# Kernel optimization log

Measured on AMD Instinct MI355X. Metric: run time of the kernel, lower is better.

The kernel has to match this reference:

```python
import jax, jax.numpy as jnp
import numpy as np

B, C, H, W = 32, 512, 32, 32
HID, MEM = 256, 256


def setup_inputs() -> dict:
    key = jax.random.key(0)
    k1, k2, k3, k4, k5, k6 = jax.random.split(key, 6)
    x = jax.random.normal(k1, (B, C, H, W), dtype=jnp.float32)
    h = jax.random.normal(k2, (B, MEM), dtype=jnp.float32)
    # conv1: 1x1 conv, no bias -> weight [HID, C]
    W_conv1 = jax.random.normal(k3, (HID, C), dtype=jnp.float32) / np.sqrt(C)
    # linear1: memory_dim -> hidden_dim, with bias
    W_lin = jax.random.normal(k4, (HID, MEM), dtype=jnp.float32) / np.sqrt(MEM)
    b_lin = jax.random.normal(k5, (HID,), dtype=jnp.float32) * 0.01
    # attention_conv: 1x1 conv hidden->1, no bias -> weight [HID]
    W_attn = jax.random.normal(k6, (HID,), dtype=jnp.float32) / np.sqrt(HID)
    return {"x": x, "h": h, "W_conv1": W_conv1, "W_lin": W_lin,
            "b_lin": b_lin, "W_attn": W_attn}


def reference(x, h, W_conv1, W_lin, b_lin, W_attn):
    # x: [B,C,H,W], h: [B,MEM]
    x2 = x.reshape(x.shape[0], x.shape[1], -1)            # [B,C,HW]
    x3 = jnp.einsum('bchw,kc->bkhw', x, W_conv1)          # 1x1 conv -> [B,HID,H,W]
    h3 = (h @ W_lin.T + b_lin)[:, :, None, None]          # [B,HID,1,1] broadcast over H,W
    a1 = jnp.tanh(x3 + h3)                                # [B,HID,H,W]
    a2 = jnp.einsum('bkhw,k->bhw', a1, W_attn).reshape(x.shape[0], -1)  # [B,HW]
    a3 = jax.nn.softmax(a2, axis=1)                       # [B,HW]
    context = jnp.einsum('bcs,bs->bc', x2, a3)            # [B,C]
    return (a3, context)
```

## Files before the change

kernel.cpp:

```cpp
#include <hip/hip_runtime.h>
#include <hip/hip_bf16.h>
#include <cmath>


typedef __bf16 bf16;
typedef __attribute__((ext_vector_type(8))) __bf16 bf16x8;
typedef __attribute__((ext_vector_type(16))) float f32x16;

__global__ __launch_bounds__(256) void prep_kernel(const float* __restrict__ h,
                                                   const float* __restrict__ Wlin,
                                                   const float* __restrict__ blin,
                                                   const float* __restrict__ Wc,
                                                   float* __restrict__ h3,
                                                   bf16* __restrict__ Whi,
                                                   bf16* __restrict__ Wlo) {
    const int tid = threadIdx.x;
    if (blockIdx.x < 32) {
        const int b = blockIdx.x;
        __shared__ float hs[256];
        hs[tid] = h[b * 256 + tid];
        __syncthreads();
        const float4* wr = (const float4*)(Wlin + (size_t)tid * 256);
        float acc = blin[tid];
        #pragma unroll 8
        for (int q = 0; q < 64; ++q) {
            float4 w = wr[q];
            float4 hv = *(const float4*)&hs[q * 4];
            acc = fmaf(w.x, hv.x, fmaf(w.y, hv.y, fmaf(w.z, hv.z, fmaf(w.w, hv.w, acc))));
        }
        h3[b * 256 + tid] = acc;
    } else {
        const int e0 = (blockIdx.x - 32) * 2048 + tid * 8;
        float4 v0 = *(const float4*)(Wc + e0);
        float4 v1 = *(const float4*)(Wc + e0 + 4);
        float vs[8] = {v0.x, v0.y, v0.z, v0.w, v1.x, v1.y, v1.z, v1.w};
        bf16x8 vh, vl;
        #pragma unroll
        for (int j = 0; j < 8; ++j) {
            bf16 hi = (bf16)vs[j];
            float r = vs[j] - (float)hi;
            vh[j] = hi;
            vl[j] = (bf16)r;
        }
        *(bf16x8*)&Whi[e0] = vh;
        *(bf16x8*)&Wlo[e0] = vl;
    }
}

__global__ __launch_bounds__(256, 2) void fused_mfma(const float* __restrict__ x,
                                                     const bf16* __restrict__ Whi,
                                                     const bf16* __restrict__ Wlo,
                                                     const float* __restrict__ h3,
                                                     const float* __restrict__ Wattn,
                                                     float* __restrict__ a2) {
    __shared__ float xbuf[2][64 * 64];
    __shared__ bf16x8 fragB[16 * 64];
    __shared__ float red2[4 * 64];

    const int tid = threadIdx.x;
    const int bid = blockIdx.x;
    const int wk = (bid & 7) * 64 + (bid >> 3);
    const int b  = wk >> 4;
    const int s0 = (wk & 15) * 64;

    const int w  = tid >> 6;
    const int l  = tid & 63;
    const int h  = l >> 5;
    const int lr = l & 31;

    const float* xb = x + ((size_t)b << 19) + s0;

    const bf16* aphi[2];
    const bf16* aplo[2];
    #pragma unroll
    for (int mf = 0; mf < 2; ++mf) {
        const size_t kr = (size_t)(64 * w + 32 * mf + lr) * 512 + 8 * h;
        aphi[mf] = Whi + kr;
        aplo[mf] = Wlo + kr;
    }

    f32x16 acc[2][2];
    #pragma unroll
    for (int mf = 0; mf < 2; ++mf)
        #pragma unroll
        for (int nf = 0; nf < 2; ++nf)
            #pragma unroll
            for (int r = 0; r < 16; ++r) acc[mf][nf][r] = 0.f;

    auto stage = [&](int tt, int nb) {
        #pragma unroll
        for (int q = 0; q < 4; ++q) {
            const float* g = xb + (size_t)(tt * 64 + 16 * q + 4 * w + (l >> 4)) * 1024
                                + 4 * (l & 15);
            __builtin_amdgcn_global_load_lds(
                (const __attribute__((address_space(1))) void*)g,
                (__attribute__((address_space(3))) void*)((char*)&xbuf[nb][0] + q * 4096 + w * 1024),
                16, 0, 0);
        }
    };

    stage(0, 0);

    #pragma unroll 1
    for (int t = 0; t < 8; ++t) {
        const int cur = t & 1;
        const int c0 = t * 64;
        __syncthreads();

        bf16x8 ah[2][4], al[2][4];
        #pragma unroll
        for (int mf = 0; mf < 2; ++mf)
            #pragma unroll
            for (int kk = 0; kk < 4; ++kk) {
                ah[mf][kk] = *(const bf16x8*)(aphi[mf] + c0 + 16 * kk);
                al[mf][kk] = *(const bf16x8*)(aplo[mf] + c0 + 16 * kk);
            }

        #pragma unroll
        for (int nf = 0; nf < 2; ++nf) {
            const int base = (16 * w + 8 * h) * 64 + 32 * nf + lr;
            float f[8];
            #pragma unroll
            for (int j = 0; j < 8; ++j) f[j] = xbuf[cur][base + j * 64];
            bf16x8 vh, vl;
            #pragma unroll
            for (int j = 0; j < 8; ++j) {
                bf16 hh = (bf16)f[j];
                vh[j] = hh;
                vl[j] = (bf16)(f[j] - (float)hh);
            }
            fragB[(w * 4 + nf * 2 + 0) * 64 + l] = vh;
            fragB[(w * 4 + nf * 2 + 1) * 64 + l] = vl;
        }
        __syncthreads();

        if (t < 7) stage(t + 1, cur ^ 1);

        #pragma unroll
        for (int kk = 0; kk < 4; ++kk) {
            bf16x8 bh0 = fragB[(kk * 4 + 0) * 64 + l];
            bf16x8 bl0 = fragB[(kk * 4 + 1) * 64 + l];
            bf16x8 bh1 = fragB[(kk * 4 + 2) * 64 + l];
            bf16x8 bl1 = fragB[(kk * 4 + 3) * 64 + l];
            #pragma unroll
            for (int mf = 0; mf < 2; ++mf) {
                acc[mf][0] = __builtin_amdgcn_mfma_f32_32x32x16_bf16(ah[mf][kk], bh0, acc[mf][0], 0, 0, 0);
                acc[mf][0] = __builtin_amdgcn_mfma_f32_32x32x16_bf16(ah[mf][kk], bl0, acc[mf][0], 0, 0, 0);
                acc[mf][0] = __builtin_amdgcn_mfma_f32_32x32x16_bf16(al[mf][kk], bh0, acc[mf][0], 0, 0, 0);
                acc[mf][1] = __builtin_amdgcn_mfma_f32_32x32x16_bf16(ah[mf][kk], bh1, acc[mf][1], 0, 0, 0);
                acc[mf][1] = __builtin_amdgcn_mfma_f32_32x32x16_bf16(ah[mf][kk], bl1, acc[mf][1], 0, 0, 0);
                acc[mf][1] = __builtin_amdgcn_mfma_f32_32x32x16_bf16(al[mf][kk], bh1, acc[mf][1], 0, 0, 0);
            }
        }
    }

    const float* h3b = h3 + b * 256;
    float part[2] = {0.f, 0.f};
    #pragma unroll
    for (int mf = 0; mf < 2; ++mf) {
        #pragma unroll
        for (int r = 0; r < 16; ++r) {
            const int k = 64 * w + 32 * mf + (r & 3) + 8 * (r >> 2) + 4 * h;
            const float hv = h3b[k];
            const float wt = Wattn[k];
            part[0] += wt * tanhf(acc[mf][0][r] + hv);
            part[1] += wt * tanhf(acc[mf][1][r] + hv);
        }
    }
    part[0] += __shfl_xor(part[0], 32, 64);
    part[1] += __shfl_xor(part[1], 32, 64);
    if (l < 32) {
        red2[w * 64 + lr]      = part[0];
        red2[w * 64 + 32 + lr] = part[1];
    }
    __syncthreads();
    if (tid < 64) {
        a2[(size_t)b * 1024 + s0 + tid] =
            red2[tid] + red2[64 + tid] + red2[128 + tid] + red2[192 + tid];
    }
}

__global__ __launch_bounds__(256) void softmax_context(const float* __restrict__ x,
                                                       const float* __restrict__ a2,
                                                       float* __restrict__ a3,
                                                       float* __restrict__ ctx) {
    __shared__ float sm[1024];
    __shared__ float red[8];
    const int tid = threadIdx.x;
    const int b = blockIdx.y, ct = blockIdx.x;
    const int wave = tid >> 6, lane = tid & 63;

    float4 v = ((const float4*)(a2 + (size_t)b * 1024))[tid];
    float m = fmaxf(fmaxf(v.x, v.y), fmaxf(v.z, v.w));
    #pragma unroll
    for (int off = 32; off >= 1; off >>= 1) m = fmaxf(m, __shfl_xor(m, off, 64));
    if (lane == 0) red[wave] = m;
    __syncthreads();
    m = fmaxf(fmaxf(red[0], red[1]), fmaxf(red[2], red[3]));
    float e0 = expf(v.x - m), e1 = expf(v.y - m), e2 = expf(v.z - m), e3 = expf(v.w - m);
    float s = e0 + e1 + e2 + e3;
    #pragma unroll
    for (int off = 32; off >= 1; off >>= 1) s += __shfl_xor(s, off, 64);
    if (lane == 0) red[4 + wave] = s;
    __syncthreads();
    s = red[4] + red[5] + red[6] + red[7];
    float inv = 1.f / s;
    float4 o = {e0 * inv, e1 * inv, e2 * inv, e3 * inv};
    ((float4*)sm)[tid] = o;
    if (ct == 0) ((float4*)(a3 + (size_t)b * 1024))[tid] = o;
    __syncthreads();

    const float* xb = x + ((size_t)b << 19);
    #pragma unroll
    for (int r = 0; r < 4; ++r) {
        int c = ct * 16 + wave * 4 + r;
        const float4* row = (const float4*)(xb + (size_t)c * 1024);
        float sum = 0.f;
        #pragma unroll
        for (int it = 0; it < 4; ++it) {
            int idx = it * 64 + lane;
            float4 xv = row[idx];
            float4 av = *(const float4*)&sm[idx * 4];
            sum = fmaf(xv.x, av.x, fmaf(xv.y, av.y, fmaf(xv.z, av.z, fmaf(xv.w, av.w, sum))));
        }
        #pragma unroll
        for (int off = 32; off >= 1; off >>= 1) sum += __shfl_xor(sum, off, 64);
        if (lane == 0) ctx[(size_t)b * 512 + c] = sum;
    }
}

extern "C" void kernel_launch(void* const* d_in, const int* in_sizes, int n_in,
                              void* d_out, int out_size, void* d_ws, size_t ws_size,
                              hipStream_t stream) {
    const float* x     = (const float*)d_in[0];
    const float* h     = (const float*)d_in[1];
    const float* Wc    = (const float*)d_in[2];
    const float* Wlin  = (const float*)d_in[3];
    const float* blin  = (const float*)d_in[4];
    const float* Wattn = (const float*)d_in[5];

    float* out = (float*)d_out;
    float* a3  = out;
    float* ctx = out + 32 * 1024;

    char* ws = (char*)d_ws;
    float* h3 = (float*)ws;
    float* a2 = (float*)(ws + 32768);
    bf16* Whi = (bf16*)(ws + 32768 + 131072);
    bf16* Wlo = (bf16*)(ws + 32768 + 131072 + 262144);

    hipLaunchKernelGGL(prep_kernel, dim3(96), dim3(256), 0, stream, h, Wlin, blin, Wc, h3, Whi, Wlo);
    hipLaunchKernelGGL(fused_mfma, dim3(512), dim3(256), 0, stream, x, Whi, Wlo, h3, Wattn, a2);
    hipLaunchKernelGGL(softmax_context, dim3(32, 32), dim3(256), 0, stream, x, a2, a3, ctx);
}
```

Before: 157.8 us.

## Drop shared B-fragment staging and barrier; convert x per wave, raise occupancy

Removes the shared fragB buffer and the second __syncthreads per K step. Each wave now reads the whole x tile from LDS for every kk, splits it into bf16 hi/lo in registers, and feeds the MFMAs directly. The next tile's global-to-LDS prefetch is issued right after the first barrier. The launch bound goes from 2 to 3 blocks per CU, using the LDS that was freed. The cost is four times the LDS reads and fp32-to-bf16 split work per block, since every wave now converts all columns instead of a quarter. Register pressure under the tighter bound could also cause spills.

```diff
diff --git a/kernel.cpp b/kernel.cpp
--- a/kernel.cpp
+++ b/kernel.cpp
@@ -47,14 +47,13 @@
     }
 }
 
-__global__ __launch_bounds__(256, 2) void fused_mfma(const float* __restrict__ x,
+__global__ __launch_bounds__(256, 3) void fused_mfma(const float* __restrict__ x,
                                                      const bf16* __restrict__ Whi,
                                                      const bf16* __restrict__ Wlo,
                                                      const float* __restrict__ h3,
                                                      const float* __restrict__ Wattn,
                                                      float* __restrict__ a2) {
     __shared__ float xbuf[2][64 * 64];
-    __shared__ bf16x8 fragB[16 * 64];
     __shared__ float red2[4 * 64];
 
     const int tid = threadIdx.x;
@@ -106,51 +105,40 @@
         const int cur = t & 1;
         const int c0 = t * 64;
         __syncthreads();
-
-        bf16x8 ah[2][4], al[2][4];
-        #pragma unroll
-        for (int mf = 0; mf < 2; ++mf)
+        if (t < 7) stage(t + 1, cur ^ 1);
+
+        #pragma unroll
+        for (int kk = 0; kk < 4; ++kk) {
+            bf16x8 ah0 = *(const bf16x8*)(aphi[0] + c0 + 16 * kk);
+            bf16x8 al0 = *(const bf16x8*)(aplo[0] + c0 + 16 * kk);
+            bf16x8 ah1 = *(const bf16x8*)(aphi[1] + c0 + 16 * kk);
+            bf16x8 al1 = *(const bf16x8*)(aplo[1] + c0 + 16 * kk);
+            bf16x8 bh[2], bl[2];
             #pragma unroll
-            for (int kk = 0; kk < 4; ++kk) {
-                ah[mf][kk] = *(const bf16x8*)(aphi[mf] + c0 + 16 * kk);
-                al[mf][kk] = *(const bf16x8*)(aplo[mf] + c0 + 16 * kk);
+            for (int nf = 0; nf < 2; ++nf) {
+                const int base = (16 * kk + 8 * h) * 64 + 32 * nf + lr;
+                float f[8];
+                #pragma unroll
+                for (int j = 0; j < 8; ++j) f[j] = xbuf[cur][base + j * 64];
+                #pragma unroll
+                for (int j = 0; j < 8; ++j) {
+                    bf16 hh = (bf16)f[j];
+                    bh[nf][j] = hh;
+                    bl[nf][j] = (bf16)(f[j] - (float)hh);
+                }
             }
-
-        #pragma unroll
-        for (int nf = 0; nf < 2; ++nf) {
-            const int base = (16 * w + 8 * h) * 64 + 32 * nf + lr;
-            float f[8];
-            #pragma unroll
-            for (int j = 0; j < 8; ++j) f[j] = xbuf[cur][base + j * 64];
-            bf16x8 vh, vl;
-            #pragma unroll
-            for (int j = 0; j < 8; ++j) {
-                bf16 hh = (bf16)f[j];
-                vh[j] = hh;
-                vl[j] = (bf16)(f[j] - (float)hh);
-            }
-            fragB[(w * 4 + nf * 2 + 0) * 64 + l] = vh;
-            fragB[(w * 4 + nf * 2 + 1) * 64 + l] = vl;
-        }
-        __syncthreads();
-
-        if (t < 7) stage(t + 1, cur ^ 1);
-
-        #pragma unroll
-        for (int kk = 0; kk < 4; ++kk) {
-            bf16x8 bh0 = fragB[(kk * 4 + 0) * 64 + l];
-            bf16x8 bl0 = fragB[(kk * 4 + 1) * 64 + l];
-            bf16x8 bh1 = fragB[(kk * 4 + 2) * 64 + l];
-            bf16x8 bl1 = fragB[(kk * 4 + 3) * 64 + l];
-            #pragma unroll
-            for (int mf = 0; mf < 2; ++mf) {
-                acc[mf][0] = __builtin_amdgcn_mfma_f32_32x32x16_bf16(ah[mf][kk], bh0, acc[mf][0], 0, 0, 0);
-                acc[mf][0] = __builtin_amdgcn_mfma_f32_32x32x16_bf16(ah[mf][kk], bl0, acc[mf][0], 0, 0, 0);
-                acc[mf][0] = __builtin_amdgcn_mfma_f32_32x32x16_bf16(al[mf][kk], bh0, acc[mf][0], 0, 0, 0);
-                acc[mf][1] = __builtin_amdgcn_mfma_f32_32x32x16_bf16(ah[mf][kk], bh1, acc[mf][1], 0, 0, 0);
-                acc[mf][1] = __builtin_amdgcn_mfma_f32_32x32x16_bf16(ah[mf][kk], bl1, acc[mf][1], 0, 0, 0);
-                acc[mf][1] = __builtin_amdgcn_mfma_f32_32x32x16_bf16(al[mf][kk], bh1, acc[mf][1], 0, 0, 0);
-            }
+            acc[0][0] = __builtin_amdgcn_mfma_f32_32x32x16_bf16(ah0, bh[0], acc[0][0], 0, 0, 0);
+            acc[0][0] = __builtin_amdgcn_mfma_f32_32x32x16_bf16(ah0, bl[0], acc[0][0], 0, 0, 0);
+            acc[0][0] = __builtin_amdgcn_mfma_f32_32x32x16_bf16(al0, bh[0], acc[0][0], 0, 0, 0);
+            acc[0][1] = __builtin_amdgcn_mfma_f32_32x32x16_bf16(ah0, bh[1], acc[0][1], 0, 0, 0);
+            acc[0][1] = __builtin_amdgcn_mfma_f32_32x32x16_bf16(ah0, bl[1], acc[0][1], 0, 0, 0);
+            acc[0][1] = __builtin_amdgcn_mfma_f32_32x32x16_bf16(al0, bh[1], acc[0][1], 0, 0, 0);
+            acc[1][0] = __builtin_amdgcn_mfma_f32_32x32x16_bf16(ah1, bh[0], acc[1][0], 0, 0, 0);
+            acc[1][0] = __builtin_amdgcn_mfma_f32_32x32x16_bf16(ah1, bl[0], acc[1][0], 0, 0, 0);
+            acc[1][0] = __builtin_amdgcn_mfma_f32_32x32x16_bf16(al1, bh[0], acc[1][0], 0, 0, 0);
+            acc[1][1] = __builtin_amdgcn_mfma_f32_32x32x16_bf16(ah1, bh[1], acc[1][1], 0, 0, 0);
+            acc[1][1] = __builtin_amdgcn_mfma_f32_32x32x16_bf16(ah1, bl[1], acc[1][1], 0, 0, 0);
+            acc[1][1] = __builtin_amdgcn_mfma_f32_32x32x16_bf16(al1, bh[1], acc[1][1], 0, 0, 0);
         }
     }
 
```

Result: faster. 154.1 us (-2.3%).
